# Optimization experiments

Hardware: AMD Instinct MI355X
Metric: run time of the kernel (lower is better)

The kernel has to match this reference:

```python
import jax, jax.numpy as jnp
import numpy as np

N = 100000   # nodes
E = 1600000  # edges (avg degree 16)
D = 128      # input feature dim
H = 128      # hidden_channels
O = 64       # out_channels


def _uniform(key, shape, fan_in):
    bound = 1.0 / np.sqrt(fan_in)
    return jax.random.uniform(key, shape, jnp.float32, -bound, bound)


def setup_inputs() -> dict:
    key = jax.random.key(0)
    ks = jax.random.split(key, 9)
    x = jax.random.normal(ks[0], (N, D), jnp.float32)
    edge_index = jax.random.randint(ks[1], (2, E), 0, N, dtype=jnp.int32)
    return {
        "x": x,
        "edge_index": edge_index,
        # layer 1: SAGEConv(D -> H): lin_l (on aggregated neighbors, with bias), lin_r (root)
        "W1l": _uniform(ks[2], (D, H), D),
        "b1": _uniform(ks[3], (H,), D),
        "W1r": _uniform(ks[4], (D, H), D),
        # layer 2: SAGEConv(H -> O)
        "W2l": _uniform(ks[5], (H, O), H),
        "b2": _uniform(ks[6], (O,), H),
        "W2r": _uniform(ks[7], (H, O), H),
    }


def sage_conv(x, edge_index, Wl, b, Wr):
    """PyG SAGEConv with mean aggregation: lin_l(mean_{j in N(i)} x_j) + lin_r(x_i)."""
    src, dst = edge_index[0], edge_index[1]
    n = x.shape[0]
    msg = x[src]                                                 # [E, D] gather
    agg = jax.ops.segment_sum(msg, dst, num_segments=n)         # [N, D] scatter-add
    cnt = jax.ops.segment_sum(jnp.ones((src.shape[0],), x.dtype), dst, num_segments=n)
    agg = agg / jnp.maximum(cnt, 1.0)[:, None]                  # mean; isolated nodes -> 0
    return agg @ Wl + b + x @ Wr


def reference(x, edge_index, W1l, b1, W1r, W2l, b2, W2r):
    h = jax.nn.relu(sage_conv(x, edge_index, W1l, b1, W1r))
    return sage_conv(h, edge_index, W2l, b2, W2r)
```

## Files before the change

### kernel.cpp

```cpp
#include <hip/hip_runtime.h>
#include <stdint.h>

#define NN 100000
#define NE 1600000
#define MAXDEG 64
#define NSLICE 8
#define SLICE_SZ 12500
#define CHUNK 6400

typedef __attribute__((ext_vector_type(8))) short short8;
typedef __attribute__((ext_vector_type(4))) float f32x4;

__device__ __forceinline__ float bflo(unsigned v) { return __uint_as_float(v << 16); }
__device__ __forceinline__ float bfhi(unsigned v) { return __uint_as_float(v & 0xffff0000u); }
__device__ __forceinline__ unsigned short f2bf(float f) {
  unsigned u = __float_as_uint(f);
  u += 0x7fff + ((u >> 16) & 1);
  return (unsigned short)(u >> 16);
}

__global__ __launch_bounds__(256) void build_buckets(const int* __restrict__ src,
                                                     const int* __restrict__ dst,
                                                     int* __restrict__ cnt,
                                                     int* __restrict__ buck) {
  const int slice = blockIdx.x & (NSLICE - 1);
  const int chunk = blockIdx.x >> 3;
  const int c0 = chunk * CHUNK;
  const int lo = slice * SLICE_SZ, hi = lo + SLICE_SZ;
  for (int e = c0 + (int)threadIdx.x * 4; e < c0 + CHUNK; e += 1024) {
    int4 d = *(const int4*)(dst + e);
    int4 s = *(const int4*)(src + e);
    if (d.x >= lo && d.x < hi) { int p = atomicAdd(&cnt[d.x], 1); if (p < MAXDEG) buck[d.x * MAXDEG + p] = s.x; }
    if (d.y >= lo && d.y < hi) { int p = atomicAdd(&cnt[d.y], 1); if (p < MAXDEG) buck[d.y * MAXDEG + p] = s.y; }
    if (d.z >= lo && d.z < hi) { int p = atomicAdd(&cnt[d.z], 1); if (p < MAXDEG) buck[d.z * MAXDEG + p] = s.z; }
    if (d.w >= lo && d.w < hi) { int p = atomicAdd(&cnt[d.w], 1); if (p < MAXDEG) buck[d.w * MAXDEG + p] = s.w; }
  }
}

__global__ __launch_bounds__(256) void to_bf16(const float* __restrict__ x,
                                               unsigned* __restrict__ xb) {
  int i = blockIdx.x * 256 + threadIdx.x;
  if (i >= NN * 32) return;
  float4 v = ((const float4*)x)[i];
  uint2 o;
  o.x = ((unsigned)f2bf(v.y) << 16) | f2bf(v.x);
  o.y = ((unsigned)f2bf(v.w) << 16) | f2bf(v.z);
  ((uint2*)xb)[i] = o;
}

__global__ __launch_bounds__(256) void transpose_w(const float* __restrict__ W1l,
                                                   const float* __restrict__ W1r,
                                                   const float* __restrict__ W2l,
                                                   const float* __restrict__ W2r,
                                                   unsigned short* __restrict__ WT1,
                                                   unsigned short* __restrict__ WT2) {
  int t = blockIdx.x * 256 + threadIdx.x;
  if (t < 128 * 256) {
    int m = t >> 8, k = t & 255;
    float v = (k < 128) ? W1l[k * 128 + m] : W1r[(k - 128) * 128 + m];
    WT1[t] = f2bf(v);
  } else {
    int i = t - 128 * 256;
    if (i < 64 * 256) {
      int m = i >> 8, k = i & 255;
      float v = (k < 128) ? W2l[k * 64 + m] : W2r[(k - 128) * 64 + m];
      WT2[i] = f2bf(v);
    }
  }
}

template <int M, bool RELU, typename OutT>
__global__ __launch_bounds__(256) void sage_fused(const unsigned* __restrict__ xb,
                                                  const int* __restrict__ cnt,
                                                  const int* __restrict__ buck,
                                                  const unsigned short* __restrict__ WT,
                                                  const float* __restrict__ bias,
                                                  OutT* __restrict__ out) {
  constexpr int LDA = 264;
  __shared__ unsigned short sA[64][LDA];

  const int t = threadIdx.x;
  const int lane = t & 63;
  const int wv = t >> 6;
  const int node0 = blockIdx.x * 64;
  const int nb = node0 + wv * 16;

  int slot[16]; unsigned xr[16]; int deg[16];
#pragma unroll
  for (int i = 0; i < 16; i++) {
    int node = nb + i;
    if (node < NN) {
      slot[i] = buck[(size_t)node * MAXDEG + lane];
      xr[i]   = xb[(size_t)node * 64 + lane];
      deg[i]  = cnt[node];
    } else { slot[i] = 0; xr[i] = 0u; deg[i] = 0; }
  }

#pragma unroll
  for (int i = 0; i < 16; i++) {
    float a0 = 0.f, a1 = 0.f;
    int dcl = min(deg[i], MAXDEG);
    if (dcl > 0) {
      int last = dcl - 1;
      for (int p = 0; p < dcl; p += 16) {
        unsigned v[16];
#pragma unroll
        for (int j = 0; j < 16; j++) {
          int s = __shfl(slot[i], min(p + j, last), 64);
          v[j] = xb[(size_t)s * 64 + lane];
        }
#pragma unroll
        for (int j = 0; j < 16; j++) {
          unsigned vj = (p + j <= last) ? v[j] : 0u;
          a0 += bflo(vj); a1 += bfhi(vj);
        }
      }
    }
    float inv = 1.f / (float)max(deg[i], 1);
    unsigned pk = ((unsigned)f2bf(a1 * inv) << 16) | f2bf(a0 * inv);
    ((unsigned*)&sA[wv * 16 + i][0])[lane]   = pk;
    ((unsigned*)&sA[wv * 16 + i][128])[lane] = xr[i];
  }

  const int m = lane & 15;
  const int q = lane >> 4;

  f32x4 acc[M / 16];
#pragma unroll
  for (int c = 0; c < M / 16; c++) acc[c] = {0.f, 0.f, 0.f, 0.f};

#pragma unroll
  for (int ks = 0; ks < 8; ks++) {
    short8 a = *(const short8*)&sA[wv * 16 + m][ks * 32 + q * 8];
#pragma unroll
    for (int c = 0; c < M / 16; c++) {
      short8 b = *(const short8*)(WT + (size_t)(c * 16 + m) * 256 + ks * 32 + q * 8);
      acc[c] = __builtin_amdgcn_mfma_f32_16x16x32_bf16(a, b, acc[c], 0, 0, 0);
    }
  }

#pragma unroll
  for (int c = 0; c < M / 16; c++) {
    int col = c * 16 + m;
    float bc = bias[col];
#pragma unroll
    for (int r = 0; r < 4; r++) {
      int lr = wv * 16 + q * 4 + r;
      float v = acc[c][r] + bc;
      if (RELU) v = fmaxf(v, 0.f);
      if constexpr (sizeof(OutT) == 2) sA[lr][col] = f2bf(v);
      else ((float*)&sA[lr][0])[col] = v;
    }
  }
#pragma unroll
  for (int it = 0; it < 4; it++) {
    int idx = it * 64 + lane;
    int rr = idx >> 4, cc = idx & 15;
    int node = node0 + wv * 16 + rr;
    if (node < NN) {
      uint4 v = *(const uint4*)((const char*)&sA[wv * 16 + rr][0] + cc * 16);
      *(uint4*)((char*)(out + (size_t)node * M) + cc * 16) = v;
    }
  }
}

extern "C" void kernel_launch(void* const* d_in, const int* in_sizes, int n_in,
                              void* d_out, int out_size, void* d_ws, size_t ws_size,
                              hipStream_t stream) {
  const float* x   = (const float*)d_in[0];
  const int*   ei  = (const int*)d_in[1];
  const float* W1l = (const float*)d_in[2];
  const float* b1  = (const float*)d_in[3];
  const float* W1r = (const float*)d_in[4];
  const float* W2l = (const float*)d_in[5];
  const float* b2  = (const float*)d_in[6];
  const float* W2r = (const float*)d_in[7];
  float* out = (float*)d_out;

  char* ws = (char*)d_ws;
  int* cnt  = (int*)ws;                                   ws += (512 << 10);
  int* buck = (int*)ws;                                   ws += (size_t)NN * MAXDEG * 4;
  unsigned* xbf = (unsigned*)ws;                          ws += (size_t)NN * 64 * 4;
  unsigned* hb = (unsigned*)ws;                           ws += (size_t)NN * 64 * 4;
  unsigned short* WT1 = (unsigned short*)ws;              ws += 128 * 256 * 2;
  unsigned short* WT2 = (unsigned short*)ws;              ws += 64 * 256 * 2;

  const int* src = ei;
  const int* dst = ei + NE;

  hipMemsetAsync(cnt, 0, (size_t)NN * 4, stream);
  build_buckets<<<NSLICE * (NE / CHUNK), 256, 0, stream>>>(src, dst, cnt, buck);
  to_bf16<<<(NN * 32 + 255) / 256, 256, 0, stream>>>(x, xbf);
  transpose_w<<<192, 256, 0, stream>>>(W1l, W1r, W2l, W2r, WT1, WT2);

  sage_fused<128, true, unsigned short><<<(NN + 63) / 64, 256, 0, stream>>>(
      xbf, cnt, buck, WT1, b1, (unsigned short*)hb);

  sage_fused<64, false, float><<<(NN + 63) / 64, 256, 0, stream>>>(
      hb, cnt, buck, WT2, b2, out);
}
```

Baseline: 377.6 us.

## Halve LDS tile, split GEMM phases, gather two neighbors per wave with 8-byte loads

The shared A tile shrinks from 64x264 to 64x136 halves by running the MFMA K-loop in two phases: aggregated neighbor means first, then the root features are reloaded into the same LDS rows for the second half. The root-feature register preload moves after aggregation, which cuts register pressure during the gather. The gather now has each half-wave read a different neighbor with 8-byte loads, and the halves are combined with a cross-lane xor shuffle. The aim is higher occupancy and more memory-level parallelism, at the cost of extra shuffles and writing the LDS tile twice. The second phase overwrites sA rows the first phase's MFMA reads with no barrier, but each wave touches only its own rows, so wave lockstep keeps this safe.

```diff
diff --git a/kernel.cpp b/kernel.cpp
--- a/kernel.cpp
+++ b/kernel.cpp
@@ -76,50 +76,61 @@
                                                   const unsigned short* __restrict__ WT,
                                                   const float* __restrict__ bias,
                                                   OutT* __restrict__ out) {
-  constexpr int LDA = 264;
-  __shared__ unsigned short sA[64][LDA];
+  __shared__ unsigned short sA[64][136];
 
   const int t = threadIdx.x;
   const int lane = t & 63;
   const int wv = t >> 6;
   const int node0 = blockIdx.x * 64;
   const int nb = node0 + wv * 16;
-
-  int slot[16]; unsigned xr[16]; int deg[16];
+  const int g = lane >> 5;
+  const int c = lane & 31;
+
+  int slot[16]; int deg[16];
 #pragma unroll
   for (int i = 0; i < 16; i++) {
     int node = nb + i;
     if (node < NN) {
       slot[i] = buck[(size_t)node * MAXDEG + lane];
-      xr[i]   = xb[(size_t)node * 64 + lane];
       deg[i]  = cnt[node];
-    } else { slot[i] = 0; xr[i] = 0u; deg[i] = 0; }
+    } else { slot[i] = 0; deg[i] = 0; }
   }
 
 #pragma unroll
   for (int i = 0; i < 16; i++) {
-    float a0 = 0.f, a1 = 0.f;
-    int dcl = min(deg[i], MAXDEG);
-    if (dcl > 0) {
-      int last = dcl - 1;
-      for (int p = 0; p < dcl; p += 16) {
-        unsigned v[16];
-#pragma unroll
-        for (int j = 0; j < 16; j++) {
-          int s = __shfl(slot[i], min(p + j, last), 64);
-          v[j] = xb[(size_t)s * 64 + lane];
+    float a0 = 0.f, a1 = 0.f, a2 = 0.f, a3 = 0.f;
+    int d = deg[i] < MAXDEG ? deg[i] : MAXDEG;
+    if (d > 0) {
+      int last = d - 1;
+      for (int p = 0; p < d; p += 16) {
+        uint2 v[8];
+#pragma unroll
+        for (int j = 0; j < 8; j++) {
+          int e = p + 2 * j + g;
+          int s = __shfl(slot[i], e < last ? e : last, 64);
+          v[j] = *(const uint2*)(xb + (size_t)s * 64 + c * 2);
         }
 #pragma unroll
-        for (int j = 0; j < 16; j++) {
-          unsigned vj = (p + j <= last) ? v[j] : 0u;
-          a0 += bflo(vj); a1 += bfhi(vj);
+        for (int j = 0; j < 8; j++) {
+          int e = p + 2 * j + g;
+          unsigned w0 = (e <= last) ? v[j].x : 0u;
+          unsigned w1 = (e <= last) ? v[j].y : 0u;
+          a0 += bflo(w0); a1 += bfhi(w0);
+          a2 += bflo(w1); a3 += bfhi(w1);
         }
       }
-    }
-    float inv = 1.f / (float)max(deg[i], 1);
-    unsigned pk = ((unsigned)f2bf(a1 * inv) << 16) | f2bf(a0 * inv);
-    ((unsigned*)&sA[wv * 16 + i][0])[lane]   = pk;
-    ((unsigned*)&sA[wv * 16 + i][128])[lane] = xr[i];
+      a0 += __shfl_xor(a0, 32, 64);
+      a1 += __shfl_xor(a1, 32, 64);
+      a2 += __shfl_xor(a2, 32, 64);
+      a3 += __shfl_xor(a3, 32, 64);
+    }
+    float inv = 1.f / (float)(deg[i] > 1 ? deg[i] : 1);
+    unsigned pk0 = ((unsigned)f2bf(a1 * inv) << 16) | f2bf(a0 * inv);
+    unsigned pk1 = ((unsigned)f2bf(a3 * inv) << 16) | f2bf(a2 * inv);
+    if (g == 0) {
+      uint2 o; o.x = pk0; o.y = pk1;
+      *(uint2*)((unsigned*)&sA[wv * 16 + i][0] + 2 * c) = o;
+    }
   }
 
   const int m = lane & 15;
@@ -127,26 +138,47 @@
 
   f32x4 acc[M / 16];
 #pragma unroll
-  for (int c = 0; c < M / 16; c++) acc[c] = {0.f, 0.f, 0.f, 0.f};
-
-#pragma unroll
-  for (int ks = 0; ks < 8; ks++) {
+  for (int cc = 0; cc < M / 16; cc++) acc[cc] = {0.f, 0.f, 0.f, 0.f};
+
+  unsigned xr[16];
+#pragma unroll
+  for (int i = 0; i < 16; i++) {
+    int node = nb + i;
+    xr[i] = (node < NN) ? xb[(size_t)node * 64 + lane] : 0u;
+  }
+
+#pragma unroll
+  for (int ks = 0; ks < 4; ks++) {
     short8 a = *(const short8*)&sA[wv * 16 + m][ks * 32 + q * 8];
 #pragma unroll
-    for (int c = 0; c < M / 16; c++) {
-      short8 b = *(const short8*)(WT + (size_t)(c * 16 + m) * 256 + ks * 32 + q * 8);
-      acc[c] = __builtin_amdgcn_mfma_f32_16x16x32_bf16(a, b, acc[c], 0, 0, 0);
-    }
-  }
-
-#pragma unroll
-  for (int c = 0; c < M / 16; c++) {
-    int col = c * 16 + m;
+    for (int cc = 0; cc < M / 16; cc++) {
+      short8 b = *(const short8*)(WT + (size_t)(cc * 16 + m) * 256 + ks * 32 + q * 8);
+      acc[cc] = __builtin_amdgcn_mfma_f32_16x16x32_bf16(a, b, acc[cc], 0, 0, 0);
+    }
+  }
+
+#pragma unroll
+  for (int i = 0; i < 16; i++)
+    ((unsigned*)&sA[wv * 16 + i][0])[lane] = xr[i];
+
+#pragma unroll
+  for (int ks = 4; ks < 8; ks++) {
+    short8 a = *(const short8*)&sA[wv * 16 + m][(ks - 4) * 32 + q * 8];
+#pragma unroll
+    for (int cc = 0; cc < M / 16; cc++) {
+      short8 b = *(const short8*)(WT + (size_t)(cc * 16 + m) * 256 + ks * 32 + q * 8);
+      acc[cc] = __builtin_amdgcn_mfma_f32_16x16x32_bf16(a, b, acc[cc], 0, 0, 0);
+    }
+  }
+
+#pragma unroll
+  for (int cc = 0; cc < M / 16; cc++) {
+    int col = cc * 16 + m;
     float bc = bias[col];
 #pragma unroll
     for (int r = 0; r < 4; r++) {
       int lr = wv * 16 + q * 4 + r;
-      float v = acc[c][r] + bc;
+      float v = acc[cc][r] + bc;
       if (RELU) v = fmaxf(v, 0.f);
       if constexpr (sizeof(OutT) == 2) sA[lr][col] = f2bf(v);
       else ((float*)&sA[lr][0])[col] = v;
@@ -155,11 +187,11 @@
 #pragma unroll
   for (int it = 0; it < 4; it++) {
     int idx = it * 64 + lane;
-    int rr = idx >> 4, cc = idx & 15;
+    int rr = idx >> 4, ck = idx & 15;
     int node = node0 + wv * 16 + rr;
     if (node < NN) {
-      uint4 v = *(const uint4*)((const char*)&sA[wv * 16 + rr][0] + cc * 16);
-      *(uint4*)((char*)(out + (size_t)node * M) + cc * 16) = v;
+      uint4 v = *(const uint4*)((const char*)&sA[wv * 16 + rr][0] + ck * 16);
+      *(uint4*)((char*)(out + (size_t)node * M) + ck * 16) = v;
     }
   }
 }
```

After: 384.2 us. About the same (+1.8%).

## Project layer-2 features before aggregation to gather 64-dim rows instead of 128

Applied to the files above, without the earlier changes.

Layer 2 now uses linearity to commute mean aggregation with the linear map. A new proj2 kernel computes h@W2l as a bf16 table and h@W2r+b2 straight into the output. A gather_add kernel then averages the 64-wide projected neighbour rows and adds them to the output. This halves the bytes gathered per edge in layer 2, at the cost of an extra kernel launch, a read-modify-write of the output, and bf16 rounding of the projected messages.

```diff
diff --git a/kernel.cpp b/kernel.cpp
--- a/kernel.cpp
+++ b/kernel.cpp
@@ -53,7 +53,7 @@
                                                    const float* __restrict__ W2l,
                                                    const float* __restrict__ W2r,
                                                    unsigned short* __restrict__ WT1,
-                                                   unsigned short* __restrict__ WT2) {
+                                                   unsigned short* __restrict__ WT2p) {
   int t = blockIdx.x * 256 + threadIdx.x;
   if (t < 128 * 256) {
     int m = t >> 8, k = t & 255;
@@ -61,10 +61,10 @@
     WT1[t] = f2bf(v);
   } else {
     int i = t - 128 * 256;
-    if (i < 64 * 256) {
-      int m = i >> 8, k = i & 255;
-      float v = (k < 128) ? W2l[k * 64 + m] : W2r[(k - 128) * 64 + m];
-      WT2[i] = f2bf(v);
+    if (i < 128 * 128) {
+      int m = i >> 7, k = i & 127;
+      float v = (m < 64) ? W2l[k * 64 + m] : W2r[k * 64 + (m - 64)];
+      WT2p[i] = f2bf(v);
     }
   }
 }
@@ -160,6 +160,130 @@
     if (node < NN) {
       uint4 v = *(const uint4*)((const char*)&sA[wv * 16 + rr][0] + cc * 16);
       *(uint4*)((char*)(out + (size_t)node * M) + cc * 16) = v;
+    }
+  }
+}
+
+__global__ __launch_bounds__(256) void proj2(const unsigned* __restrict__ hb,
+                                             const unsigned short* __restrict__ WTp,
+                                             const float* __restrict__ b2,
+                                             unsigned* __restrict__ p,
+                                             float* __restrict__ out) {
+  __shared__ unsigned short sA[64][136];
+  const int lane = threadIdx.x & 63, wv = threadIdx.x >> 6;
+  const int node0 = blockIdx.x * 64, nb = node0 + wv * 16;
+
+#pragma unroll
+  for (int i = 0; i < 16; i++) {
+    int node = nb + i;
+    unsigned v = (node < NN) ? hb[(size_t)node * 64 + lane] : 0u;
+    ((unsigned*)&sA[wv * 16 + i][0])[lane] = v;
+  }
+
+  const int m = lane & 15, q = lane >> 4;
+  f32x4 acc[8];
+#pragma unroll
+  for (int cc = 0; cc < 8; cc++) acc[cc] = {0.f, 0.f, 0.f, 0.f};
+#pragma unroll
+  for (int ks = 0; ks < 4; ks++) {
+    short8 a = *(const short8*)&sA[wv * 16 + m][ks * 32 + q * 8];
+#pragma unroll
+    for (int cc = 0; cc < 8; cc++) {
+      short8 b = *(const short8*)(WTp + (size_t)(cc * 16 + m) * 128 + ks * 32 + q * 8);
+      acc[cc] = __builtin_amdgcn_mfma_f32_16x16x32_bf16(a, b, acc[cc], 0, 0, 0);
+    }
+  }
+
+#pragma unroll
+  for (int cc = 0; cc < 4; cc++) {
+    int col = cc * 16 + m;
+#pragma unroll
+    for (int r = 0; r < 4; r++) {
+      int lr = wv * 16 + q * 4 + r;
+      sA[lr][col] = f2bf(acc[cc][r]);
+    }
+  }
+#pragma unroll
+  for (int it = 0; it < 2; it++) {
+    int idx = it * 64 + lane;
+    int rr = idx >> 3, ck = idx & 7;
+    int node = nb + rr;
+    if (node < NN) {
+      uint4 v = *(const uint4*)((const char*)&sA[wv * 16 + rr][0] + ck * 16);
+      *(uint4*)((char*)(p + (size_t)node * 32) + ck * 16) = v;
+    }
+  }
+#pragma unroll
+  for (int cc = 4; cc < 8; cc++) {
+    int col = (cc - 4) * 16 + m;
+    float bc = b2[col];
+#pragma unroll
+    for (int r = 0; r < 4; r++) {
+      int lr = wv * 16 + q * 4 + r;
+      ((float*)&sA[lr][0])[col] = acc[cc][r] + bc;
+    }
+  }
+#pragma unroll
+  for (int it = 0; it < 4; it++) {
+    int idx = it * 64 + lane;
+    int rr = idx >> 4, ck = idx & 15;
+    int node = nb + rr;
+    if (node < NN) {
+      uint4 v = *(const uint4*)((const char*)&sA[wv * 16 + rr][0] + ck * 16);
+      *(uint4*)((char*)(out + (size_t)node * 64) + ck * 16) = v;
+    }
+  }
+}
+
+__global__ __launch_bounds__(256) void gather_add(const unsigned* __restrict__ p,
+                                                  const int* __restrict__ cnt,
+                                                  const int* __restrict__ buck,
+                                                  float* __restrict__ out) {
+  const int lane = threadIdx.x & 63, wv = threadIdx.x >> 6;
+  const int nb = blockIdx.x * 64 + wv * 16;
+  const int g = lane >> 5, c = lane & 31;
+
+  int slot[16]; int deg[16];
+#pragma unroll
+  for (int i = 0; i < 16; i++) {
+    int node = nb + i;
+    if (node < NN) {
+      slot[i] = buck[(size_t)node * MAXDEG + lane];
+      deg[i]  = cnt[node];
+    } else { slot[i] = 0; deg[i] = 0; }
+  }
+
+#pragma unroll
+  for (int i = 0; i < 16; i++) {
+    float a0 = 0.f, a1 = 0.f;
+    int d = min(deg[i], MAXDEG);
+    if (d > 0) {
+      int last = d - 1;
+      for (int pp = 0; pp < d; pp += 16) {
+        unsigned v[8];
+#pragma unroll
+        for (int j = 0; j < 8; j++) {
+          int e = pp + 2 * j + g;
+          int s = __shfl(slot[i], e < last ? e : last, 64);
+          v[j] = p[(size_t)s * 32 + c];
+        }
+#pragma unroll
+        for (int j = 0; j < 8; j++) {
+          int e = pp + 2 * j + g;
+          unsigned w = (e <= last) ? v[j] : 0u;
+          a0 += bflo(w); a1 += bfhi(w);
+        }
+      }
+      a0 += __shfl_xor(a0, 32, 64);
+      a1 += __shfl_xor(a1, 32, 64);
+    }
+    int node = nb + i;
+    if (node < NN && lane < 32) {
+      float inv = 1.f / (float)max(deg[i], 1);
+      float2* fp = (float2*)(out + (size_t)node * 64 + 2 * c);
+      float2 tv = *fp;
+      tv.x += a0 * inv; tv.y += a1 * inv;
+      *fp = tv;
     }
   }
 }
@@ -183,7 +307,8 @@
   unsigned* xbf = (unsigned*)ws;                          ws += (size_t)NN * 64 * 4;
   unsigned* hb = (unsigned*)ws;                           ws += (size_t)NN * 64 * 4;
   unsigned short* WT1 = (unsigned short*)ws;              ws += 128 * 256 * 2;
-  unsigned short* WT2 = (unsigned short*)ws;              ws += 64 * 256 * 2;
+  unsigned short* WT2p = (unsigned short*)ws;             ws += 128 * 128 * 2;
+  unsigned* ptab = xbf;
 
   const int* src = ei;
   const int* dst = ei + NE;
@@ -191,11 +316,12 @@
   hipMemsetAsync(cnt, 0, (size_t)NN * 4, stream);
   build_buckets<<<NSLICE * (NE / CHUNK), 256, 0, stream>>>(src, dst, cnt, buck);
   to_bf16<<<(NN * 32 + 255) / 256, 256, 0, stream>>>(x, xbf);
-  transpose_w<<<192, 256, 0, stream>>>(W1l, W1r, W2l, W2r, WT1, WT2);
+  transpose_w<<<192, 256, 0, stream>>>(W1l, W1r, W2l, W2r, WT1, WT2p);
 
   sage_fused<128, true, unsigned short><<<(NN + 63) / 64, 256, 0, stream>>>(
       xbf, cnt, buck, WT1, b1, (unsigned short*)hb);
 
-  sage_fused<64, false, float><<<(NN + 63) / 64, 256, 0, stream>>>(
-      hb, cnt, buck, WT2, b2, out);
-}
+  proj2<<<(NN + 63) / 64, 256, 0, stream>>>(hb, WT2p, b2, ptab, out);
+
+  gather_add<<<(NN + 63) / 64, 256, 0, stream>>>(ptab, cnt, buck, out);
+}
```

After: 388.0 us. 2.8% more time.
